# Kernel optimization log

Measured on AMD Instinct MI355X. Metric: run time of the kernel, lower is better.

The kernel has to match this reference:

```python
import jax, jax.numpy as jnp
import numpy as np

NEIGHBOR_NUM = 32  # init kwarg neighbor_num

B, N, C = 64, 512, 1024

def setup_inputs() -> dict:
    key = jax.random.key(0)
    x = jax.random.normal(key, (B, N, C), dtype=jnp.float32)
    return {"x": x}

def reference(x):
    # si = x @ x^T (detached in the original -> stop_gradient)
    si = jax.lax.stop_gradient(x)
    si = jnp.einsum('bic,bjc->bij', si, si)  # (b, n, n)
    # k-th largest value per row as threshold
    topv, _ = jax.lax.top_k(si, NEIGHBOR_NUM)          # (b, n, k)
    threshold = topv[..., -1:]                          # (b, n, 1)
    adj = (si >= threshold).astype(si.dtype)            # (b, n, n)
    # normalize_digraph: D^{-1/2} A D^{-1/2} with D = row-degree diag
    node_degrees = adj.sum(axis=-1)                     # (b, n)
    degs_inv_sqrt = node_degrees ** (-0.5)              # (b, n)
    # diag(d) @ A @ diag(d) == d_i * A_ij * d_j
    norm_A = degs_inv_sqrt[:, :, None] * adj * degs_inv_sqrt[:, None, :]
    return norm_A
```

## Files before the change

### kernel.cpp

```cpp
#include <hip/hip_runtime.h>
#include <hip/hip_bf16.h>
#include <math.h>

#define B 64
#define N 512
#define C 1024
#define K_NEIGH 32
#define DELTA 0.625f
#define BISECT_ITERS 14

typedef __attribute__((ext_vector_type(8))) _Float16 half8;
typedef __attribute__((ext_vector_type(4))) float f32x4;

__global__ __launch_bounds__(256) void gemm_f16(const float* __restrict__ x,
                                                float* __restrict__ S) {
    __shared__ half8 Ah[512], Bh[512];

    const int b = blockIdx.x;
    int p = blockIdx.y;
    int ti = 0;
    while (p >= (4 - ti)) { p -= (4 - ti); ti++; }
    const int tj = ti + p;
    const int row0A = ti * 128;
    const int row0B = tj * 128;
    const float* xb = x + (size_t)b * N * C;

    const int t    = threadIdx.x;
    const int w    = t >> 6;
    const int lane = t & 63;
    const int quad = lane >> 4;
    const int lid  = lane & 15;
    const int wr   = (w >> 1) * 64;
    const int wc   = (w & 1) * 64;

    const int srow = t >> 1;
    const int sg   = (t & 1) * 2;

    f32x4 acc[4][4];
#pragma unroll
    for (int r = 0; r < 4; r++)
#pragma unroll
        for (int c = 0; c < 4; c++)
#pragma unroll
            for (int e = 0; e < 4; e++) acc[r][c][e] = 0.f;

    for (int kt = 0; kt < C; kt += 32) {
        {
            const float* pa = xb + (size_t)(row0A + srow) * C + kt + sg * 8;
            float4 f0 = ((const float4*)pa)[0];
            float4 f1 = ((const float4*)pa)[1];
            float4 f2 = ((const float4*)pa)[2];
            float4 f3 = ((const float4*)pa)[3];
            half8 g0, g1;
            g0[0] = (_Float16)f0.x; g0[1] = (_Float16)f0.y; g0[2] = (_Float16)f0.z; g0[3] = (_Float16)f0.w;
            g0[4] = (_Float16)f1.x; g0[5] = (_Float16)f1.y; g0[6] = (_Float16)f1.z; g0[7] = (_Float16)f1.w;
            g1[0] = (_Float16)f2.x; g1[1] = (_Float16)f2.y; g1[2] = (_Float16)f2.z; g1[3] = (_Float16)f2.w;
            g1[4] = (_Float16)f3.x; g1[5] = (_Float16)f3.y; g1[6] = (_Float16)f3.z; g1[7] = (_Float16)f3.w;
            Ah[sg * 128 + srow]       = g0;
            Ah[(sg + 1) * 128 + srow] = g1;
        }
        {
            const float* pb = xb + (size_t)(row0B + srow) * C + kt + sg * 8;
            float4 f0 = ((const float4*)pb)[0];
            float4 f1 = ((const float4*)pb)[1];
            float4 f2 = ((const float4*)pb)[2];
            float4 f3 = ((const float4*)pb)[3];
            half8 g0, g1;
            g0[0] = (_Float16)f0.x; g0[1] = (_Float16)f0.y; g0[2] = (_Float16)f0.z; g0[3] = (_Float16)f0.w;
            g0[4] = (_Float16)f1.x; g0[5] = (_Float16)f1.y; g0[6] = (_Float16)f1.z; g0[7] = (_Float16)f1.w;
            g1[0] = (_Float16)f2.x; g1[1] = (_Float16)f2.y; g1[2] = (_Float16)f2.z; g1[3] = (_Float16)f2.w;
            g1[4] = (_Float16)f3.x; g1[5] = (_Float16)f3.y; g1[6] = (_Float16)f3.z; g1[7] = (_Float16)f3.w;
            Bh[sg * 128 + srow]       = g0;
            Bh[(sg + 1) * 128 + srow] = g1;
        }
        __syncthreads();

        half8 vb[4];
#pragma unroll
        for (int c = 0; c < 4; c++) vb[c] = Bh[quad * 128 + wc + c * 16 + lid];
#pragma unroll
        for (int r = 0; r < 4; r++) {
            half8 va = Ah[quad * 128 + wr + r * 16 + lid];
#pragma unroll
            for (int c = 0; c < 4; c++)
                acc[r][c] = __builtin_amdgcn_mfma_f32_16x16x32_f16(va, vb[c], acc[r][c], 0, 0, 0);
        }
        __syncthreads();
    }

    float* Sb = S + (size_t)b * N * N;
#pragma unroll
    for (int r = 0; r < 4; r++) {
#pragma unroll
        for (int c = 0; c < 4; c++) {
#pragma unroll
            for (int e = 0; e < 4; e++) {
                const int grow = row0A + wr + r * 16 + quad * 4 + e;
                const int gcol = row0B + wc + c * 16 + lid;
                const float vv = acc[r][c][e];
                Sb[(size_t)grow * N + gcol] = vv;
                if (ti != tj) Sb[(size_t)gcol * N + grow] = vv;
            }
        }
    }
}

__global__ __launch_bounds__(256) void thresh_mask(const float* __restrict__ S,
                                                   const float* __restrict__ x,
                                                   unsigned long long* __restrict__ masks,
                                                   float* __restrict__ dinv) {
    const int row  = blockIdx.x * 4 + (threadIdx.x >> 6);
    const int lane = threadIdx.x & 63;
    const float* Srow = S + (size_t)row * N;

    float v0[8];
#pragma unroll
    for (int k = 0; k < 8; k++) v0[k] = Srow[lane + 64 * k];

    float lo = -1400.f, hi = 1400.f;
    for (int it = 0; it < BISECT_ITERS; it++) {
        const float mid = 0.5f * (lo + hi);
        int c = 0;
#pragma unroll
        for (int k = 0; k < 8; k++) c += __popcll(__ballot(v0[k] > mid));
        if (c >= K_NEIGH) lo = mid; else hi = mid;
    }
    const float P   = 0.5f * (lo + hi);
    const float hiB = P + DELTA, loB = P - DELTA;

    int cA = 0;
#pragma unroll
    for (int k = 0; k < 8; k++) cA += __popcll(__ballot(v0[k] > hiB));
    const int m_need = K_NEIGH - cA;

    int cnt = 0, myj = -1;
#pragma unroll
    for (int kq = 0; kq < 8; kq++) {
        unsigned long long bm = __ballot(v0[kq] >= loB && v0[kq] <= hiB);
        while (bm) {
            int bl = __ffsll(bm) - 1;
            bm &= bm - 1;
            if (cnt == lane) myj = bl + 64 * kq;
            cnt++;
        }
    }
    const int nc = cnt < 64 ? cnt : 64;

    const int bb_ = row >> 9, ii = row & (N - 1);
    const float* xi = x + ((size_t)bb_ * N + ii) * C;
    float4 ai[4];
#pragma unroll
    for (int q = 0; q < 4; q++) ai[q] = *(const float4*)(xi + q * 256 + lane * 4);

    float ex = -INFINITY;
    for (int c2 = 0; c2 < nc; c2++) {
        const int j = __shfl(myj, c2);
        const float* xj = x + ((size_t)bb_ * N + j) * C;
        float s = 0.f;
#pragma unroll
        for (int q = 0; q < 4; q++) {
            float4 bv = *(const float4*)(xj + q * 256 + lane * 4);
            s = fmaf(ai[q].x, bv.x, s);
            s = fmaf(ai[q].y, bv.y, s);
            s = fmaf(ai[q].z, bv.z, s);
            s = fmaf(ai[q].w, bv.w, s);
        }
#pragma unroll
        for (int off = 32; off > 0; off >>= 1) s += __shfl_xor(s, off);
        if (lane == c2) ex = s;
    }

    float val = ex, T = -INFINITY;
    for (int it = 0; it < m_need; it++) {
        float M = val;
#pragma unroll
        for (int off = 32; off > 0; off >>= 1) M = fmaxf(M, __shfl_xor(M, off));
        T = M;
        unsigned long long ball = __ballot(val == M);
        int first = __ffsll(ball) - 1;
        if (lane == first) val = -INFINITY;
    }
    const int dec = (lane < nc && ex >= T) ? 1 : 0;

    int bits[8];
#pragma unroll
    for (int kq = 0; kq < 8; kq++) bits[kq] = (v0[kq] > hiB) ? 1 : 0;
    for (int c2 = 0; c2 < nc; c2++) {
        int j = __shfl(myj, c2);
        int d = __shfl(dec, c2);
        if ((j & 63) == lane) bits[j >> 6] = d;
    }

    unsigned long long msk[8];
    int deg = 0;
#pragma unroll
    for (int kq = 0; kq < 8; kq++) {
        msk[kq] = __ballot(bits[kq] != 0);
        deg += __popcll(msk[kq]);
    }
    if (lane == 0) {
#pragma unroll
        for (int kq = 0; kq < 8; kq++) masks[(size_t)row * 8 + kq] = msk[kq];
        dinv[row] = rsqrtf((float)deg);
    }
}

__global__ __launch_bounds__(256) void scale_adj(float* __restrict__ Sout,
                                                 const unsigned long long* __restrict__ masks,
                                                 const float* __restrict__ dinv) {
    const int idx = blockIdx.x * 256 + threadIdx.x;
    const int jq = idx & 127;
    const int i  = (idx >> 7) & (N - 1);
    const int b  = idx >> 16;
    const int row = (b << 9) | i;
    const int j0 = jq * 4;

    const unsigned long long mk = masks[(size_t)row * 8 + (j0 >> 6)];
    const float di = dinv[row];
    float4 dj = ((const float4*)dinv)[(b << 7) | jq];

    float4 o;
    o.x = ((mk >> ((j0 + 0) & 63)) & 1ull) ? di * dj.x : 0.f;
    o.y = ((mk >> ((j0 + 1) & 63)) & 1ull) ? di * dj.y : 0.f;
    o.z = ((mk >> ((j0 + 2) & 63)) & 1ull) ? di * dj.z : 0.f;
    o.w = ((mk >> ((j0 + 3) & 63)) & 1ull) ? di * dj.w : 0.f;
    ((float4*)Sout)[idx] = o;
}

extern "C" void kernel_launch(void* const* d_in, const int* in_sizes, int n_in,
                              void* d_out, int out_size, void* d_ws, size_t ws_size,
                              hipStream_t stream) {
    const float* x = (const float*)d_in[0];
    float* out = (float*)d_out;
    unsigned long long* masks = (unsigned long long*)d_ws;
    float* dinv = (float*)(masks + (size_t)B * N * 8);

    dim3 g1(B, 10);
    gemm_f16<<<g1, 256, 0, stream>>>(x, out);
    thresh_mask<<<B * N / 4, 256, 0, stream>>>(out, x, masks, dinv);
    const int total4 = B * N * N / 4;
    scale_adj<<<total4 / 256, 256, 0, stream>>>(out, masks, dinv);
}
```

Baseline: 329.1 us.

## Double-buffer GEMM LDS tiles, drop symmetric tile reuse, vectorize threshold row loads

The GEMM now prefetches the next K-slice from global memory into registers while MFMAs run on the current LDS buffer, using two LDS buffers and one barrier per iteration. The symmetric-tile trick (10 tiles with a transposed scattered store) is replaced by computing all 16 tiles with only coalesced row-major stores, trading about 60% more MFMA and load work for no strided transpose writes. The threshold kernel loads each row with contiguous float4 reads, so each lane owns 8 consecutive columns, and builds the 64-bit masks with byte packing and shuffles instead of eight ballots.

```diff
diff --git a/kernel.cpp b/kernel.cpp
--- a/kernel.cpp
+++ b/kernel.cpp
@@ -8,19 +8,25 @@
 #define K_NEIGH 32
 #define DELTA 0.625f
 #define BISECT_ITERS 14
+#define NITER (C / 32)
 
 typedef __attribute__((ext_vector_type(8))) _Float16 half8;
 typedef __attribute__((ext_vector_type(4))) float f32x4;
 
+__device__ inline half8 cvt16(float4 f0, float4 f1) {
+    half8 g;
+    g[0] = (_Float16)f0.x; g[1] = (_Float16)f0.y; g[2] = (_Float16)f0.z; g[3] = (_Float16)f0.w;
+    g[4] = (_Float16)f1.x; g[5] = (_Float16)f1.y; g[6] = (_Float16)f1.z; g[7] = (_Float16)f1.w;
+    return g;
+}
+
 __global__ __launch_bounds__(256) void gemm_f16(const float* __restrict__ x,
                                                 float* __restrict__ S) {
-    __shared__ half8 Ah[512], Bh[512];
-
-    const int b = blockIdx.x;
-    int p = blockIdx.y;
-    int ti = 0;
-    while (p >= (4 - ti)) { p -= (4 - ti); ti++; }
-    const int tj = ti + p;
+    __shared__ half8 Abuf[2][512], Bbuf[2][512];
+
+    const int b  = blockIdx.x;
+    const int ti = blockIdx.y >> 2;
+    const int tj = blockIdx.y & 3;
     const int row0A = ti * 128;
     const int row0B = tj * 128;
     const float* xb = x + (size_t)b * N * C;
@@ -35,6 +41,8 @@
 
     const int srow = t >> 1;
     const int sg   = (t & 1) * 2;
+    const float* pA = xb + (size_t)(row0A + srow) * C + sg * 8;
+    const float* pB = xb + (size_t)(row0B + srow) * C + sg * 8;
 
     f32x4 acc[4][4];
 #pragma unroll
@@ -44,48 +52,48 @@
 #pragma unroll
             for (int e = 0; e < 4; e++) acc[r][c][e] = 0.f;
 
-    for (int kt = 0; kt < C; kt += 32) {
-        {
-            const float* pa = xb + (size_t)(row0A + srow) * C + kt + sg * 8;
-            float4 f0 = ((const float4*)pa)[0];
-            float4 f1 = ((const float4*)pa)[1];
-            float4 f2 = ((const float4*)pa)[2];
-            float4 f3 = ((const float4*)pa)[3];
-            half8 g0, g1;
-            g0[0] = (_Float16)f0.x; g0[1] = (_Float16)f0.y; g0[2] = (_Float16)f0.z; g0[3] = (_Float16)f0.w;
-            g0[4] = (_Float16)f1.x; g0[5] = (_Float16)f1.y; g0[6] = (_Float16)f1.z; g0[7] = (_Float16)f1.w;
-            g1[0] = (_Float16)f2.x; g1[1] = (_Float16)f2.y; g1[2] = (_Float16)f2.z; g1[3] = (_Float16)f2.w;
-            g1[4] = (_Float16)f3.x; g1[5] = (_Float16)f3.y; g1[6] = (_Float16)f3.z; g1[7] = (_Float16)f3.w;
-            Ah[sg * 128 + srow]       = g0;
-            Ah[(sg + 1) * 128 + srow] = g1;
-        }
-        {
-            const float* pb = xb + (size_t)(row0B + srow) * C + kt + sg * 8;
-            float4 f0 = ((const float4*)pb)[0];
-            float4 f1 = ((const float4*)pb)[1];
-            float4 f2 = ((const float4*)pb)[2];
-            float4 f3 = ((const float4*)pb)[3];
-            half8 g0, g1;
-            g0[0] = (_Float16)f0.x; g0[1] = (_Float16)f0.y; g0[2] = (_Float16)f0.z; g0[3] = (_Float16)f0.w;
-            g0[4] = (_Float16)f1.x; g0[5] = (_Float16)f1.y; g0[6] = (_Float16)f1.z; g0[7] = (_Float16)f1.w;
-            g1[0] = (_Float16)f2.x; g1[1] = (_Float16)f2.y; g1[2] = (_Float16)f2.z; g1[3] = (_Float16)f2.w;
-            g1[4] = (_Float16)f3.x; g1[5] = (_Float16)f3.y; g1[6] = (_Float16)f3.z; g1[7] = (_Float16)f3.w;
-            Bh[sg * 128 + srow]       = g0;
-            Bh[(sg + 1) * 128 + srow] = g1;
-        }
-        __syncthreads();
+    float4 fa[4], fb[4];
+    {
+        const float4* qa = (const float4*)pA;
+        const float4* qb = (const float4*)pB;
+#pragma unroll
+        for (int i = 0; i < 4; i++) { fa[i] = qa[i]; fb[i] = qb[i]; }
+        Abuf[0][sg * 128 + srow]       = cvt16(fa[0], fa[1]);
+        Abuf[0][(sg + 1) * 128 + srow] = cvt16(fa[2], fa[3]);
+        Bbuf[0][sg * 128 + srow]       = cvt16(fb[0], fb[1]);
+        Bbuf[0][(sg + 1) * 128 + srow] = cvt16(fb[2], fb[3]);
+    }
+    __syncthreads();
+
+    int p = 0;
+    for (int kt = 0; kt < NITER; kt++) {
+        if (kt + 1 < NITER) {
+            const float4* qa = (const float4*)(pA + (kt + 1) * 32);
+            const float4* qb = (const float4*)(pB + (kt + 1) * 32);
+#pragma unroll
+            for (int i = 0; i < 4; i++) { fa[i] = qa[i]; fb[i] = qb[i]; }
+        }
 
         half8 vb[4];
 #pragma unroll
-        for (int c = 0; c < 4; c++) vb[c] = Bh[quad * 128 + wc + c * 16 + lid];
+        for (int c = 0; c < 4; c++) vb[c] = Bbuf[p][quad * 128 + wc + c * 16 + lid];
 #pragma unroll
         for (int r = 0; r < 4; r++) {
-            half8 va = Ah[quad * 128 + wr + r * 16 + lid];
+            half8 va = Abuf[p][quad * 128 + wr + r * 16 + lid];
 #pragma unroll
             for (int c = 0; c < 4; c++)
                 acc[r][c] = __builtin_amdgcn_mfma_f32_16x16x32_f16(va, vb[c], acc[r][c], 0, 0, 0);
         }
+
+        if (kt + 1 < NITER) {
+            const int q = p ^ 1;
+            Abuf[q][sg * 128 + srow]       = cvt16(fa[0], fa[1]);
+            Abuf[q][(sg + 1) * 128 + srow] = cvt16(fa[2], fa[3]);
+            Bbuf[q][sg * 128 + srow]       = cvt16(fb[0], fb[1]);
+            Bbuf[q][(sg + 1) * 128 + srow] = cvt16(fb[2], fb[3]);
+        }
         __syncthreads();
+        p ^= 1;
     }
 
     float* Sb = S + (size_t)b * N * N;
@@ -97,9 +105,7 @@
             for (int e = 0; e < 4; e++) {
                 const int grow = row0A + wr + r * 16 + quad * 4 + e;
                 const int gcol = row0B + wc + c * 16 + lid;
-                const float vv = acc[r][c][e];
-                Sb[(size_t)grow * N + gcol] = vv;
-                if (ti != tj) Sb[(size_t)gcol * N + grow] = vv;
+                Sb[(size_t)grow * N + gcol] = acc[r][c][e];
             }
         }
     }
@@ -113,9 +119,9 @@
     const int lane = threadIdx.x & 63;
     const float* Srow = S + (size_t)row * N;
 
-    float v0[8];
-#pragma unroll
-    for (int k = 0; k < 8; k++) v0[k] = Srow[lane + 64 * k];
+    float4 a0 = ((const float4*)Srow)[lane * 2];
+    float4 a1 = ((const float4*)Srow)[lane * 2 + 1];
+    float v0[8] = {a0.x, a0.y, a0.z, a0.w, a1.x, a1.y, a1.z, a1.w};
 
     float lo = -1400.f, hi = 1400.f;
     for (int it = 0; it < BISECT_ITERS; it++) {
@@ -140,7 +146,7 @@
         while (bm) {
             int bl = __ffsll(bm) - 1;
             bm &= bm - 1;
-            if (cnt == lane) myj = bl + 64 * kq;
+            if (cnt == lane) myj = bl * 8 + kq;
             cnt++;
         }
     }
@@ -182,27 +188,26 @@
     }
     const int dec = (lane < nc && ex >= T) ? 1 : 0;
 
-    int bits[8];
-#pragma unroll
-    for (int kq = 0; kq < 8; kq++) bits[kq] = (v0[kq] > hiB) ? 1 : 0;
+    unsigned byte = 0;
+#pragma unroll
+    for (int k = 0; k < 8; k++) byte |= (v0[k] > hiB) ? (1u << k) : 0u;
     for (int c2 = 0; c2 < nc; c2++) {
         int j = __shfl(myj, c2);
         int d = __shfl(dec, c2);
-        if ((j & 63) == lane) bits[j >> 6] = d;
-    }
-
-    unsigned long long msk[8];
-    int deg = 0;
-#pragma unroll
-    for (int kq = 0; kq < 8; kq++) {
-        msk[kq] = __ballot(bits[kq] != 0);
-        deg += __popcll(msk[kq]);
-    }
-    if (lane == 0) {
-#pragma unroll
-        for (int kq = 0; kq < 8; kq++) masks[(size_t)row * 8 + kq] = msk[kq];
-        dinv[row] = rsqrtf((float)deg);
-    }
+        if ((j >> 3) == lane) byte |= (unsigned)d << (j & 7);
+    }
+
+    unsigned long long part = (unsigned long long)byte << ((lane & 7) * 8);
+    part |= __shfl_xor(part, 1);
+    part |= __shfl_xor(part, 2);
+    part |= __shfl_xor(part, 4);
+
+    int deg = __popc(byte);
+#pragma unroll
+    for (int off = 32; off > 0; off >>= 1) deg += __shfl_xor(deg, off);
+
+    if ((lane & 7) == 0) masks[(size_t)row * 8 + (lane >> 3)] = part;
+    if (lane == 0) dinv[row] = rsqrtf((float)deg);
 }
 
 __global__ __launch_bounds__(256) void scale_adj(float* __restrict__ Sout,
@@ -235,7 +240,7 @@
     unsigned long long* masks = (unsigned long long*)d_ws;
     float* dinv = (float*)(masks + (size_t)B * N * 8);
 
-    dim3 g1(B, 10);
+    dim3 g1(B, 16);
     gemm_f16<<<g1, 256, 0, stream>>>(x, out);
     thresh_mask<<<B * N / 4, 256, 0, stream>>>(out, x, masks, dinv);
     const int total4 = B * N * N / 4;
```

Measured after the change: 370.6 us. +12.6%, slower.

## Fuse Gram GEMM with threshold selection via fp16 pre-conversion and LDS-resident scores

Applied to the files above, without the earlier changes.

Adds a pre-pass that converts x to fp16, writing it into the output buffer as scratch. A new fused kernel computes a 64-row strip of the similarity matrix per block, with double-buffered async global-to-LDS loads. It keeps the scores in LDS as fp16 and runs the bisection and top-k threshold logic directly from LDS. This removes the round trip of the full fp32 similarity matrix through global memory. In exchange it drops the symmetric-tile saving, so GEMM work is duplicated, and it serialises 16 rows per wave. Rounding scores to fp16 before bisection may also affect threshold correctness near the band edges.

```diff
diff --git a/kernel.cpp b/kernel.cpp
--- a/kernel.cpp
+++ b/kernel.cpp
@@ -8,200 +8,215 @@
 #define K_NEIGH 32
 #define DELTA 0.625f
 #define BISECT_ITERS 14
+#define NKT (C / 32)
+#define SLD 68
 
 typedef __attribute__((ext_vector_type(8))) _Float16 half8;
 typedef __attribute__((ext_vector_type(4))) float f32x4;
 
-__global__ __launch_bounds__(256) void gemm_f16(const float* __restrict__ x,
-                                                float* __restrict__ S) {
-    __shared__ half8 Ah[512], Bh[512];
-
-    const int b = blockIdx.x;
-    int p = blockIdx.y;
-    int ti = 0;
-    while (p >= (4 - ti)) { p -= (4 - ti); ti++; }
-    const int tj = ti + p;
-    const int row0A = ti * 128;
-    const int row0B = tj * 128;
-    const float* xb = x + (size_t)b * N * C;
-
-    const int t    = threadIdx.x;
-    const int w    = t >> 6;
-    const int lane = t & 63;
-    const int quad = lane >> 4;
-    const int lid  = lane & 15;
-    const int wr   = (w >> 1) * 64;
-    const int wc   = (w & 1) * 64;
-
-    const int srow = t >> 1;
-    const int sg   = (t & 1) * 2;
-
-    f32x4 acc[4][4];
+__device__ __forceinline__ void async_copy16(void* lds, const void* gmem) {
+    __builtin_amdgcn_global_load_lds(
+        (const __attribute__((address_space(1))) unsigned int*)gmem,
+        (__attribute__((address_space(3))) unsigned int*)lds,
+        16, 0, 0);
+}
+
+__global__ __launch_bounds__(256) void cvt_f16(const float* __restrict__ x,
+                                               _Float16* __restrict__ xh) {
+    const int t = blockIdx.x * 256 + threadIdx.x;
+    float4 a = ((const float4*)x)[t * 2];
+    float4 b = ((const float4*)x)[t * 2 + 1];
+    half8 h;
+    h[0] = (_Float16)a.x; h[1] = (_Float16)a.y; h[2] = (_Float16)a.z; h[3] = (_Float16)a.w;
+    h[4] = (_Float16)b.x; h[5] = (_Float16)b.y; h[6] = (_Float16)b.z; h[7] = (_Float16)b.w;
+    ((half8*)xh)[t] = h;
+}
+
+__global__ __launch_bounds__(256, 2) void gemm_thresh(
+        const _Float16* __restrict__ xh, const float* __restrict__ x,
+        unsigned long long* __restrict__ masks, float* __restrict__ dinv) {
+    extern __shared__ char smem[];
+    _Float16* Sl = (_Float16*)smem;
+
+    const int rg = blockIdx.x;
+    const int b  = blockIdx.y;
+    const int t = threadIdx.x, w = t >> 6, lane = t & 63;
+    const int quad = lane >> 4, lid = lane & 15;
+    const int wc = w * 128;
+
+    const char* xb = (const char*)(xh + (size_t)b * N * C);
+    const int srow16 = lane & 15;
+    const int sqtr   = lane >> 4;
+
+    f32x4 acc[4][8];
 #pragma unroll
     for (int r = 0; r < 4; r++)
 #pragma unroll
-        for (int c = 0; c < 4; c++)
+        for (int c = 0; c < 8; c++)
 #pragma unroll
             for (int e = 0; e < 4; e++) acc[r][c][e] = 0.f;
 
-    for (int kt = 0; kt < C; kt += 32) {
-        {
-            const float* pa = xb + (size_t)(row0A + srow) * C + kt + sg * 8;
-            float4 f0 = ((const float4*)pa)[0];
-            float4 f1 = ((const float4*)pa)[1];
-            float4 f2 = ((const float4*)pa)[2];
-            float4 f3 = ((const float4*)pa)[3];
-            half8 g0, g1;
-            g0[0] = (_Float16)f0.x; g0[1] = (_Float16)f0.y; g0[2] = (_Float16)f0.z; g0[3] = (_Float16)f0.w;
-            g0[4] = (_Float16)f1.x; g0[5] = (_Float16)f1.y; g0[6] = (_Float16)f1.z; g0[7] = (_Float16)f1.w;
-            g1[0] = (_Float16)f2.x; g1[1] = (_Float16)f2.y; g1[2] = (_Float16)f2.z; g1[3] = (_Float16)f2.w;
-            g1[4] = (_Float16)f3.x; g1[5] = (_Float16)f3.y; g1[6] = (_Float16)f3.z; g1[7] = (_Float16)f3.w;
-            Ah[sg * 128 + srow]       = g0;
-            Ah[(sg + 1) * 128 + srow] = g1;
-        }
-        {
-            const float* pb = xb + (size_t)(row0B + srow) * C + kt + sg * 8;
-            float4 f0 = ((const float4*)pb)[0];
-            float4 f1 = ((const float4*)pb)[1];
-            float4 f2 = ((const float4*)pb)[2];
-            float4 f3 = ((const float4*)pb)[3];
-            half8 g0, g1;
-            g0[0] = (_Float16)f0.x; g0[1] = (_Float16)f0.y; g0[2] = (_Float16)f0.z; g0[3] = (_Float16)f0.w;
-            g0[4] = (_Float16)f1.x; g0[5] = (_Float16)f1.y; g0[6] = (_Float16)f1.z; g0[7] = (_Float16)f1.w;
-            g1[0] = (_Float16)f2.x; g1[1] = (_Float16)f2.y; g1[2] = (_Float16)f2.z; g1[3] = (_Float16)f2.w;
-            g1[4] = (_Float16)f3.x; g1[5] = (_Float16)f3.y; g1[6] = (_Float16)f3.z; g1[7] = (_Float16)f3.w;
-            Bh[sg * 128 + srow]       = g0;
-            Bh[(sg + 1) * 128 + srow] = g1;
+#pragma unroll
+    for (int i = 0; i < 8; i++) {
+        const int m = w * 8 + i;
+        const char* src = xb + (size_t)(m * 16 + srow16) * 2048 + sqtr * 16;
+        async_copy16(smem + m * 1024 + lane * 16, src);
+    }
+    __syncthreads();
+
+    for (int kt = 0; kt < NKT; kt++) {
+        const int pb = kt & 1;
+        if (kt + 1 < NKT) {
+            char* dbuf = smem + ((kt + 1) & 1) * 32768;
+#pragma unroll
+            for (int i = 0; i < 8; i++) {
+                const int m = w * 8 + i;
+                const char* src = xb + (size_t)(m * 16 + srow16) * 2048
+                                  + (kt + 1) * 64 + sqtr * 16;
+                async_copy16(dbuf + m * 1024 + lane * 16, src);
+            }
+        }
+        const half8* sb = (const half8*)(smem + pb * 32768);
+        half8 vb[8];
+#pragma unroll
+        for (int c = 0; c < 8; c++) vb[c] = sb[(w * 8 + c) * 64 + quad * 16 + lid];
+#pragma unroll
+        for (int r = 0; r < 4; r++) {
+            half8 va = sb[(rg * 4 + r) * 64 + quad * 16 + lid];
+#pragma unroll
+            for (int c = 0; c < 8; c++)
+                acc[r][c] = __builtin_amdgcn_mfma_f32_16x16x32_f16(va, vb[c], acc[r][c], 0, 0, 0);
         }
         __syncthreads();
-
-        half8 vb[4];
-#pragma unroll
-        for (int c = 0; c < 4; c++) vb[c] = Bh[quad * 128 + wc + c * 16 + lid];
-#pragma unroll
-        for (int r = 0; r < 4; r++) {
-            half8 va = Ah[quad * 128 + wr + r * 16 + lid];
-#pragma unroll
-            for (int c = 0; c < 4; c++)
-                acc[r][c] = __builtin_amdgcn_mfma_f32_16x16x32_f16(va, vb[c], acc[r][c], 0, 0, 0);
-        }
-        __syncthreads();
-    }
-
-    float* Sb = S + (size_t)b * N * N;
+    }
+
+    union H4 { _Float16 h[4]; unsigned long long u; };
 #pragma unroll
     for (int r = 0; r < 4; r++) {
 #pragma unroll
-        for (int c = 0; c < 4; c++) {
-#pragma unroll
-            for (int e = 0; e < 4; e++) {
-                const int grow = row0A + wr + r * 16 + quad * 4 + e;
-                const int gcol = row0B + wc + c * 16 + lid;
-                const float vv = acc[r][c][e];
-                Sb[(size_t)grow * N + gcol] = vv;
-                if (ti != tj) Sb[(size_t)gcol * N + grow] = vv;
-            }
-        }
-    }
-}
-
-__global__ __launch_bounds__(256) void thresh_mask(const float* __restrict__ S,
-                                                   const float* __restrict__ x,
-                                                   unsigned long long* __restrict__ masks,
-                                                   float* __restrict__ dinv) {
-    const int row  = blockIdx.x * 4 + (threadIdx.x >> 6);
-    const int lane = threadIdx.x & 63;
-    const float* Srow = S + (size_t)row * N;
-
-    float v0[8];
-#pragma unroll
-    for (int k = 0; k < 8; k++) v0[k] = Srow[lane + 64 * k];
-
-    float lo = -1400.f, hi = 1400.f;
-    for (int it = 0; it < BISECT_ITERS; it++) {
-        const float mid = 0.5f * (lo + hi);
-        int c = 0;
-#pragma unroll
-        for (int k = 0; k < 8; k++) c += __popcll(__ballot(v0[k] > mid));
-        if (c >= K_NEIGH) lo = mid; else hi = mid;
-    }
-    const float P   = 0.5f * (lo + hi);
-    const float hiB = P + DELTA, loB = P - DELTA;
-
-    int cA = 0;
-#pragma unroll
-    for (int k = 0; k < 8; k++) cA += __popcll(__ballot(v0[k] > hiB));
-    const int m_need = K_NEIGH - cA;
-
-    int cnt = 0, myj = -1;
-#pragma unroll
-    for (int kq = 0; kq < 8; kq++) {
-        unsigned long long bm = __ballot(v0[kq] >= loB && v0[kq] <= hiB);
-        while (bm) {
-            int bl = __ffsll(bm) - 1;
-            bm &= bm - 1;
-            if (cnt == lane) myj = bl + 64 * kq;
-            cnt++;
-        }
-    }
-    const int nc = cnt < 64 ? cnt : 64;
-
-    const int bb_ = row >> 9, ii = row & (N - 1);
-    const float* xi = x + ((size_t)bb_ * N + ii) * C;
-    float4 ai[4];
-#pragma unroll
-    for (int q = 0; q < 4; q++) ai[q] = *(const float4*)(xi + q * 256 + lane * 4);
-
-    float ex = -INFINITY;
-    for (int c2 = 0; c2 < nc; c2++) {
-        const int j = __shfl(myj, c2);
-        const float* xj = x + ((size_t)bb_ * N + j) * C;
-        float s = 0.f;
-#pragma unroll
-        for (int q = 0; q < 4; q++) {
-            float4 bv = *(const float4*)(xj + q * 256 + lane * 4);
-            s = fmaf(ai[q].x, bv.x, s);
-            s = fmaf(ai[q].y, bv.y, s);
-            s = fmaf(ai[q].z, bv.z, s);
-            s = fmaf(ai[q].w, bv.w, s);
-        }
-#pragma unroll
-        for (int off = 32; off > 0; off >>= 1) s += __shfl_xor(s, off);
-        if (lane == c2) ex = s;
-    }
-
-    float val = ex, T = -INFINITY;
-    for (int it = 0; it < m_need; it++) {
-        float M = val;
-#pragma unroll
-        for (int off = 32; off > 0; off >>= 1) M = fmaxf(M, __shfl_xor(M, off));
-        T = M;
-        unsigned long long ball = __ballot(val == M);
-        int first = __ffsll(ball) - 1;
-        if (lane == first) val = -INFINITY;
-    }
-    const int dec = (lane < nc && ex >= T) ? 1 : 0;
-
-    int bits[8];
-#pragma unroll
-    for (int kq = 0; kq < 8; kq++) bits[kq] = (v0[kq] > hiB) ? 1 : 0;
-    for (int c2 = 0; c2 < nc; c2++) {
-        int j = __shfl(myj, c2);
-        int d = __shfl(dec, c2);
-        if ((j & 63) == lane) bits[j >> 6] = d;
-    }
-
-    unsigned long long msk[8];
-    int deg = 0;
-#pragma unroll
-    for (int kq = 0; kq < 8; kq++) {
-        msk[kq] = __ballot(bits[kq] != 0);
-        deg += __popcll(msk[kq]);
-    }
-    if (lane == 0) {
-#pragma unroll
-        for (int kq = 0; kq < 8; kq++) masks[(size_t)row * 8 + kq] = msk[kq];
-        dinv[row] = rsqrtf((float)deg);
+        for (int c = 0; c < 8; c++) {
+            const int col  = wc + c * 16 + lid;
+            const int row0 = r * 16 + quad * 4;
+            H4 pk;
+            pk.h[0] = (_Float16)acc[r][c][0];
+            pk.h[1] = (_Float16)acc[r][c][1];
+            pk.h[2] = (_Float16)acc[r][c][2];
+            pk.h[3] = (_Float16)acc[r][c][3];
+            *(unsigned long long*)(&Sl[col * SLD + row0]) = pk.u;
+        }
+    }
+    __syncthreads();
+
+    const float* xB = x + (size_t)b * N * C;
+    for (int lr = w * 16; lr < w * 16 + 16; lr++) {
+        float v0[8];
+#pragma unroll
+        for (int k = 0; k < 8; k++)
+            v0[k] = (float)Sl[(lane + 64 * k) * SLD + lr];
+
+        float lo = -1400.f, hi = 1400.f;
+        for (int it = 0; it < BISECT_ITERS; it++) {
+            const float mid = 0.5f * (lo + hi);
+            int c = 0;
+#pragma unroll
+            for (int k = 0; k < 8; k++) c += __popcll(__ballot(v0[k] > mid));
+            if (c >= K_NEIGH) lo = mid; else hi = mid;
+        }
+        const float P   = 0.5f * (lo + hi);
+        const float hiB = P + DELTA, loB = P - DELTA;
+
+        int cA = 0;
+#pragma unroll
+        for (int k = 0; k < 8; k++) cA += __popcll(__ballot(v0[k] > hiB));
+        const int m_need = K_NEIGH - cA;
+
+        int cnt = 0, myj = -1;
+#pragma unroll
+        for (int kq = 0; kq < 8; kq++) {
+            unsigned long long bm = __ballot(v0[kq] >= loB && v0[kq] <= hiB);
+            while (bm) {
+                int bl = __ffsll(bm) - 1;
+                bm &= bm - 1;
+                if (cnt == lane) myj = bl + 64 * kq;
+                cnt++;
+            }
+        }
+        const int nc = cnt < 64 ? cnt : 64;
+
+        const int gi = rg * 64 + lr;
+        const float* xi = xB + (size_t)gi * C;
+        float4 ai[4];
+#pragma unroll
+        for (int q = 0; q < 4; q++) ai[q] = *(const float4*)(xi + q * 256 + lane * 4);
+
+        float ex = -INFINITY;
+        for (int g = 0; g < nc; g += 4) {
+            float4 bv[4][4];
+            int jn[4];
+#pragma unroll
+            for (int u = 0; u < 4; u++) {
+                jn[u] = __shfl(myj, (g + u < nc) ? (g + u) : g);
+                const float* xj = xB + (size_t)jn[u] * C;
+#pragma unroll
+                for (int q = 0; q < 4; q++)
+                    bv[u][q] = *(const float4*)(xj + q * 256 + lane * 4);
+            }
+#pragma unroll
+            for (int u = 0; u < 4; u++) {
+                if (g + u < nc) {
+                    float s = 0.f;
+#pragma unroll
+                    for (int q = 0; q < 4; q++) {
+                        s = fmaf(ai[q].x, bv[u][q].x, s);
+                        s = fmaf(ai[q].y, bv[u][q].y, s);
+                        s = fmaf(ai[q].z, bv[u][q].z, s);
+                        s = fmaf(ai[q].w, bv[u][q].w, s);
+                    }
+#pragma unroll
+                    for (int off = 32; off > 0; off >>= 1) s += __shfl_xor(s, off);
+                    if (lane == g + u) ex = s;
+                }
+            }
+        }
+
+        float val = ex, T = -INFINITY;
+        for (int it = 0; it < m_need; it++) {
+            float M = val;
+#pragma unroll
+            for (int off = 32; off > 0; off >>= 1) M = fmaxf(M, __shfl_xor(M, off));
+            T = M;
+            unsigned long long ball = __ballot(val == M);
+            int first = __ffsll(ball) - 1;
+            if (lane == first) val = -INFINITY;
+        }
+        const int dec = (lane < nc && ex >= T) ? 1 : 0;
+
+        int bits[8];
+#pragma unroll
+        for (int k = 0; k < 8; k++) bits[k] = (v0[k] > hiB) ? 1 : 0;
+        for (int c2 = 0; c2 < nc; c2++) {
+            int j = __shfl(myj, c2);
+            int d = __shfl(dec, c2);
+            if (lane == (j & 63)) {
+#pragma unroll
+                for (int k = 0; k < 8; k++)
+                    if (k == (j >> 6)) bits[k] = d;
+            }
+        }
+
+        unsigned long long msk[8];
+        int deg = 0;
+#pragma unroll
+        for (int k = 0; k < 8; k++) {
+            msk[k] = __ballot(bits[k] != 0);
+            deg += __popcll(msk[k]);
+        }
+        if (lane == 0) {
+            const size_t row_g = (size_t)b * N + gi;
+#pragma unroll
+            for (int k = 0; k < 8; k++) masks[row_g * 8 + k] = msk[k];
+            dinv[row_g] = rsqrtf((float)deg);
+        }
     }
 }
 
@@ -232,12 +247,12 @@
                               hipStream_t stream) {
     const float* x = (const float*)d_in[0];
     float* out = (float*)d_out;
+    _Float16* xh = (_Float16*)d_out;
     unsigned long long* masks = (unsigned long long*)d_ws;
-    float* dinv = (float*)(masks + (size_t)B * N * 8);
-
-    dim3 g1(B, 10);
-    gemm_f16<<<g1, 256, 0, stream>>>(x, out);
-    thresh_mask<<<B * N / 4, 256, 0, stream>>>(out, x, masks, dinv);
+    float* dinvp = (float*)(masks + (size_t)B * N * 8);
+
+    cvt_f16<<<(B * N * C / 8) / 256, 256, 0, stream>>>(x, xh);
+    gemm_thresh<<<dim3(8, B), 256, 69632, stream>>>(xh, x, masks, dinvp);
     const int total4 = B * N * N / 4;
-    scale_adj<<<total4 / 256, 256, 0, stream>>>(out, masks, dinv);
-}
+    scale_adj<<<total4 / 256, 256, 0, stream>>>(out, masks, dinvp);
+}
```

New measurement: 412.2 us. 1.25x slower.
